# Optimization experiments

Measured on AMD Instinct MI355X. Metric: run time of the kernel, lower is better.

The kernel has to match this reference:

```python
import jax, jax.numpy as jnp
import numpy as np

N_HEAD = 6
NEG_INF = -1e9


def _structural_masks(adj, distance):
    """Build the 6 per-head structural masks (B, 6, L, L) bool.

    Heads: [self-loop only, 1-hop (adj), 2-hop reachable, distance<=2,
            distance<=3, global]. Inferred from the 6-signal docstring;
    preprocess_adj adds self loops and binarizes.
    """
    B, L, _ = adj.shape
    eye = jnp.eye(L, dtype=bool)[None]                      # (1, L, L)
    a1 = (adj > 0) | eye                                    # 1-hop + self
    a1f = a1.astype(jnp.float32)
    a2 = (jnp.einsum('blm,bmn->bln', a1f, a1f) > 0)         # 2-hop reachable
    d2 = distance <= 2
    d3 = distance <= 3
    full = jnp.ones((B, L, L), dtype=bool)
    return jnp.stack([jnp.broadcast_to(eye, (B, L, L)), a1, a2, d2, d3, full], axis=1)


def setup_inputs() -> dict:
    key = jax.random.key(0)
    k1, k2, k3, k4, k5 = jax.random.split(key, 5)
    B, L, C = 8, 1024, 768
    x = jax.random.normal(k1, (B, L, C), dtype=jnp.float32)
    adj = jax.random.randint(k2, (B, L, L), 0, 2, dtype=jnp.int32)
    distance = jax.random.randint(k3, (B, L, L), 0, 9, dtype=jnp.int32)
    w_qkv = jax.random.normal(k4, (3 * C, C), dtype=jnp.float32) * 0.02
    w_proj = jax.random.normal(k5, (C, C), dtype=jnp.float32) * 0.02
    return {"x": x, "adj": adj, "distance": distance, "w_qkv": w_qkv, "w_proj": w_proj}


def reference(x, adj, distance, w_qkv, w_proj):
    B, L, C = x.shape
    H = N_HEAD
    d = C // H
    scale = jnp.sqrt(jnp.float32(d))

    qkv = x @ w_qkv.T                                       # (B, L, 3C)
    q, k, v = jnp.split(qkv, 3, axis=-1)
    q = q.reshape(B, L, H, d).transpose(0, 2, 1, 3)         # (B, H, L, d)
    k = k.reshape(B, L, H, d).transpose(0, 2, 1, 3)
    v = v.reshape(B, L, H, d).transpose(0, 2, 1, 3)

    score = jnp.einsum('bhld,bhmd->bhlm', q, k) / scale     # (B, H, L, L)
    pe = _structural_masks(adj, distance)                   # (B, H, L, L) bool
    score = jnp.where(pe, score, NEG_INF)                   # masked_fill of bias
    attn = jax.nn.softmax(score, axis=-1)
    out = jnp.einsum('bhlm,bhmd->bhld', attn, v)            # (B, H, L, d)
    out = out.transpose(0, 2, 1, 3).reshape(B, L, C)
    return out @ w_proj.T
```

## Files before the change

### kernel.cpp

```cpp
#include <hip/hip_runtime.h>

typedef unsigned short ushort_t;
typedef unsigned int uint_t;
typedef unsigned long long u64;
typedef __attribute__((ext_vector_type(8))) short bf16x8;
typedef __attribute__((ext_vector_type(4))) float f32x4;
typedef __attribute__((ext_vector_type(16))) float f32x16;
typedef __attribute__((ext_vector_type(4))) uint_t u32x4;

#define B_ 8
#define L_ 1024
#define C_ 768
#define H_ 6
#define D_ 128
#define BH_ 48
#define NEGINF (-1e9f)
#define THR_ 8.0f

#define AS1 __attribute__((address_space(1)))
#define AS3 __attribute__((address_space(3)))

__device__ __forceinline__ ushort_t f2bf(float f) {
  uint_t u = __builtin_bit_cast(uint_t, f);
  u += 0x7fffu + ((u >> 16) & 1u);
  return (ushort_t)(u >> 16);
}
__device__ __forceinline__ float bf2f(ushort_t s) {
  uint_t u = ((uint_t)s) << 16;
  return __builtin_bit_cast(float, u);
}

__global__ void cvt_f32_bf16(const float* __restrict__ in, ushort_t* __restrict__ out, int n8) {
  int i = blockIdx.x * 256 + threadIdx.x;
  if (i >= n8) return;
  const float4* p = (const float4*)in + (size_t)i * 2;
  float4 a = p[0], b = p[1];
  uint4 r;
  r.x = (uint_t)f2bf(a.x) | ((uint_t)f2bf(a.y) << 16);
  r.y = (uint_t)f2bf(a.z) | ((uint_t)f2bf(a.w) << 16);
  r.z = (uint_t)f2bf(b.x) | ((uint_t)f2bf(b.y) << 16);
  r.w = (uint_t)f2bf(b.z) | ((uint_t)f2bf(b.w) << 16);
  ((uint4*)out)[i] = r;
}

__global__ __launch_bounds__(256)
void pack_masks(const int* __restrict__ adj, const int* __restrict__ dist,
                u64* __restrict__ a1p, u64* __restrict__ d2p, u64* __restrict__ d3p) {
  int l = blockIdx.x, b = blockIdx.y, t = threadIdx.x;
  size_t base = ((size_t)b * L_ + l) * L_;
  size_t rb = ((size_t)b * L_ + l) * 16;
  #pragma unroll
  for (int it = 0; it < 4; ++it) {
    int c = it * 256 + t;
    int av = adj[base + c];
    int dv = dist[base + c];
    u64 m1 = __ballot((av > 0) || (c == l));
    u64 m2 = __ballot(dv <= 2);
    u64 m3 = __ballot(dv <= 3);
    if ((t & 63) == 0) {
      int w = it * 4 + (t >> 6);
      a1p[rb + w] = m1; d2p[rb + w] = m2; d3p[rb + w] = m3;
    }
  }
}

__global__ __launch_bounds__(64)
void hop2(const u64* __restrict__ a1p, u64* __restrict__ a2p) {
  int tid = blockIdx.x * 64 + threadIdx.x;
  int b = tid >> 10;
  size_t rb = (size_t)tid * 16;
  u64 row[16], acc[16];
  #pragma unroll
  for (int j = 0; j < 16; ++j) { row[j] = a1p[rb + j]; acc[j] = 0ULL; }
  bool done = false;
  #pragma unroll
  for (int mw = 0; mw < 16; ++mw) {
    if (done) continue;
    u64 bits = row[mw];
    while (bits) {
      int tz = __builtin_ctzll(bits); bits &= bits - 1;
      const u64* src = a1p + (((size_t)b << 10) + (mw << 6) + tz) * 16;
      u64 band = ~0ULL;
      #pragma unroll
      for (int j = 0; j < 16; ++j) { acc[j] |= src[j]; band &= acc[j]; }
      if (band == ~0ULL) { done = true; break; }
    }
  }
  #pragma unroll
  for (int j = 0; j < 16; ++j) a2p[rb + j] = acc[j];
}

template<int EPI>
__global__ __launch_bounds__(256)
void gemm_bt(const ushort_t* __restrict__ A, const ushort_t* __restrict__ Bm,
             int N, int K,
             ushort_t* __restrict__ qo, ushort_t* __restrict__ ko,
             ushort_t* __restrict__ vTo, ushort_t* __restrict__ vo,
             float* __restrict__ fo) {
  __shared__ __align__(16) ushort_t As[128 * 64];
  __shared__ __align__(16) ushort_t Bs[128 * 64];
  int t = threadIdx.x;
  int lane = t & 63, lo = lane & 15, hi = lane >> 4;
  int wv = t >> 6, wm = wv >> 1, wn = wv & 1;

  int gx = gridDim.x;
  int nwg = gx * gridDim.y;
  int orig = blockIdx.y * gx + blockIdx.x;
  int cpx = nwg >> 3;
  int wg = (orig & 7) * cpx + (orig >> 3);
  int n0 = (wg % gx) * 128;
  int m0 = (wg / gx) * 128;

  f32x4 acc[4][4];
  #pragma unroll
  for (int mi = 0; mi < 4; ++mi)
    #pragma unroll
    for (int ni = 0; ni < 4; ++ni) acc[mi][ni] = (f32x4){0.f, 0.f, 0.f, 0.f};

  for (int kt = 0; kt < K; kt += 64) {
    #pragma unroll
    for (int i = 0; i < 4; ++i) {
      int u = i * 256 + t;
      int row = u >> 3, c16 = u & 7;
      int sc = c16 ^ (row & 7);
      __builtin_amdgcn_global_load_lds(
          (const AS1 void*)(A + ((size_t)(m0 + row) * K + kt + sc * 8)),
          (AS3 void*)&As[(size_t)u * 8], 16, 0, 0);
      __builtin_amdgcn_global_load_lds(
          (const AS1 void*)(Bm + ((size_t)(n0 + row) * K + kt + sc * 8)),
          (AS3 void*)&Bs[(size_t)u * 8], 16, 0, 0);
    }
    __syncthreads();
    #pragma unroll
    for (int kks = 0; kks < 2; ++kks) {
      bf16x8 af[4], bfr[4];
      #pragma unroll
      for (int mi = 0; mi < 4; ++mi) {
        int r = wm * 64 + mi * 16 + lo;
        af[mi] = *(const bf16x8*)&As[r * 64 + (((kks * 4 + hi) ^ (r & 7)) * 8)];
      }
      #pragma unroll
      for (int ni = 0; ni < 4; ++ni) {
        int r = wn * 64 + ni * 16 + lo;
        bfr[ni] = *(const bf16x8*)&Bs[r * 64 + (((kks * 4 + hi) ^ (r & 7)) * 8)];
      }
      #pragma unroll
      for (int mi = 0; mi < 4; ++mi)
        #pragma unroll
        for (int ni = 0; ni < 4; ++ni)
          acc[mi][ni] = __builtin_amdgcn_mfma_f32_16x16x32_bf16(af[mi], bfr[ni], acc[mi][ni], 0, 0, 0);
    }
    __syncthreads();
  }

  if (EPI == 1) {
    #pragma unroll
    for (int mi = 0; mi < 4; ++mi) {
      int rbase = m0 + wm * 64 + mi * 16 + hi * 4;
      #pragma unroll
      for (int ni = 0; ni < 4; ++ni) {
        int c = n0 + wn * 64 + ni * 16 + lo;
        f32x4 v = acc[mi][ni];
        #pragma unroll
        for (int j = 0; j < 4; ++j)
          fo[(size_t)(rbase + j) * N + c] = v[j];
      }
    }
    return;
  }
  int sec = n0 / 768;
  if (sec < 2) {
    #pragma unroll
    for (int mi = 0; mi < 4; ++mi) {
      int rbase = m0 + wm * 64 + mi * 16 + hi * 4;
      #pragma unroll
      for (int ni = 0; ni < 4; ++ni) {
        int cc = n0 - sec * 768 + wn * 64 + ni * 16 + lo;
        int hh = cc >> 7, dd = cc & 127;
        f32x4 v = acc[mi][ni];
        #pragma unroll
        for (int j = 0; j < 4; ++j) {
          int r = rbase + j;
          int b = r >> 10, l = r & 1023;
          size_t bh = (size_t)(b * H_ + hh);
          if (sec == 0) qo[(bh * L_ + l) * D_ + dd] = f2bf(v[j] * 0.08838834764831845f);
          else          ko[(bh * L_ + l) * D_ + dd] = f2bf(v[j]);
        }
      }
    }
    return;
  }
  int hh = (n0 - 1536) >> 7;
  int b = m0 >> 10, l0 = m0 & 1023;
  size_t bh = (size_t)(b * H_ + hh);
  if (hh == 0) {
    #pragma unroll
    for (int mi = 0; mi < 4; ++mi) {
      int lb = wm * 64 + mi * 16 + hi * 4;
      #pragma unroll
      for (int ni = 0; ni < 4; ++ni) {
        int dd = wn * 64 + ni * 16 + lo;
        f32x4 v = acc[mi][ni];
        #pragma unroll
        for (int j = 0; j < 4; ++j)
          vo[(bh * L_ + l0 + lb + j) * D_ + dd] = f2bf(v[j]);
      }
    }
    return;
  }
  #pragma unroll
  for (int mi = 0; mi < 4; ++mi) {
    int lb = wm * 64 + mi * 16 + hi * 4;
    #pragma unroll
    for (int ni = 0; ni < 4; ++ni) {
      int dd = wn * 64 + ni * 16 + lo;
      ushort_t* base = (dd < 64) ? As : Bs;
      f32x4 v = acc[mi][ni];
      #pragma unroll
      for (int j = 0; j < 4; ++j) {
        int byte = (((dd & 63) * 256 + (lb + j) * 2)) ^ ((dd & 7) << 4);
        *(ushort_t*)((char*)base + byte) = f2bf(v[j]);
      }
    }
  }
  __syncthreads();
  #pragma unroll
  for (int i = 0; i < 8; ++i) {
    int u = i * 256 + t;
    int ddl = u >> 4, c16 = u & 15;
    const ushort_t* base = (ddl < 64) ? As : Bs;
    int byte = (((ddl & 63) * 256 + c16 * 16)) ^ ((ddl & 7) << 4);
    bf16x8 val = *(const bf16x8*)((const char*)base + byte);
    *(bf16x8*)(vTo + (bh * D_ + ddl) * L_ + l0 + c16 * 8) = val;
  }
}

__global__ __launch_bounds__(512)
void attn_kernel(const ushort_t* __restrict__ q, const ushort_t* __restrict__ k,
                 const ushort_t* __restrict__ vT, const ushort_t* __restrict__ v,
                 ushort_t* __restrict__ obf,
                 ushort_t* __restrict__ np0, ushort_t* __restrict__ np1,
                 ushort_t* __restrict__ np2, ushort_t* __restrict__ np3,
                 float* __restrict__ ml,
                 const u64* __restrict__ a1p, const u64* __restrict__ a2p,
                 const u64* __restrict__ d2p, const u64* __restrict__ d3p) {
  __shared__ __align__(16) ushort_t Ks[2][32 * 128];
  __shared__ __align__(16) ushort_t Vs[2][128 * 32];
  int t = threadIdx.x;
  int lane = t & 63, lo32 = lane & 31, hi2 = (lane >> 5) & 1, wv = t >> 6;
  int bh = blockIdx.x, qt = blockIdx.y, quar = blockIdx.z;
  int b = bh / H_, h = bh - b * H_;
  int qbase = qt * 256;
  int qw = qbase + wv * 32;
  int kvb = quar * 256;

  if (h == 0) {
    if (quar) return;
    const ushort_t* vp0 = v + ((size_t)bh * L_ + qbase) * D_;
    ushort_t* op0 = obf + ((size_t)b * L_ + qbase) * C_;
    #pragma unroll
    for (int it = 0; it < 8; ++it) {
      int u = it * 512 + t;
      int r = u >> 4, c = (u & 15) * 8;
      *(bf16x8*)(op0 + (size_t)r * C_ + c) = *(const bf16x8*)(vp0 + (size_t)r * D_ + c);
    }
    return;
  }

  const ushort_t* qp = q + (size_t)bh * L_ * D_;
  const ushort_t* kp = k + (size_t)bh * L_ * D_ + (size_t)kvb * D_;
  const ushort_t* vp = vT + (size_t)bh * D_ * L_ + kvb;

  bf16x8 qf[8];
  #pragma unroll
  for (int dt = 0; dt < 8; ++dt)
    qf[dt] = *(const bf16x8*)(qp + (size_t)(qw + lo32) * D_ + dt * 16 + hi2 * 8);

  const u64* mp = (h == 1) ? a1p : (h == 2) ? a2p : (h == 3) ? d2p : d3p;
  bool full = (h == 5);
  const u64* mrow = mp + ((size_t)b * L_ + qw + lo32) * 16 + quar * 4;

  float m_run = NEGINF, l_run = 0.f;
  f32x16 acc[4];
  #pragma unroll
  for (int dt = 0; dt < 4; ++dt)
    #pragma unroll
    for (int r = 0; r < 16; ++r) acc[dt][r] = 0.f;

  auto stage = [&](int buf, int ch) {
    int kc0 = ch * 32;
    {
      int row = t >> 4, c16 = t & 15;
      int sc = c16 ^ (row & 15);
      __builtin_amdgcn_global_load_lds(
          (const AS1 void*)(kp + (size_t)(kc0 + row) * D_ + sc * 8),
          (AS3 void*)&Ks[buf][(size_t)t * 8], 16, 0, 0);
    }
    {
      int row = t >> 2, c16 = t & 3;
      int sc = c16 ^ (row & 3);
      __builtin_amdgcn_global_load_lds(
          (const AS1 void*)(vp + (size_t)row * L_ + kc0 + sc * 8),
          (AS3 void*)&Vs[buf][(size_t)t * 8], 16, 0, 0);
    }
  };

  stage(0, 0);
  u64 mw_cur = full ? 0ULL : mrow[0];
  u64 mw_nxt = 0ULL;
  __syncthreads();

  for (int ch = 0; ch < 8; ++ch) {
    int cur = ch & 1;
    if (ch < 7) stage(cur ^ 1, ch + 1);
    if (!full && (ch & 1) == 0 && (ch >> 1) + 1 < 4)
      mw_nxt = mrow[(ch >> 1) + 1];

    const ushort_t* ks = &Ks[cur][0];
    const ushort_t* vs = &Vs[cur][0];
    uint_t mbits = full ? 0xffffffffu : (uint_t)(mw_cur >> ((ch & 1) * 32));

    f32x16 sacc;
    #pragma unroll
    for (int r = 0; r < 16; ++r) sacc[r] = 0.f;
    __builtin_amdgcn_s_setprio(1);
    #pragma unroll
    for (int dt = 0; dt < 8; ++dt) {
      int c16 = (dt * 2 + hi2) ^ (lo32 & 15);
      bf16x8 kf = *(const bf16x8*)&ks[lo32 * 128 + c16 * 8];
      sacc = __builtin_amdgcn_mfma_f32_32x32x16_bf16(kf, qf[dt], sacc, 0, 0, 0);
    }
    __builtin_amdgcn_s_setprio(0);

    float sv[16];
    #pragma unroll
    for (int r = 0; r < 16; ++r) {
      int shift = (r & 3) + 8 * (r >> 2) + hi2 * 4;
      sv[r] = ((mbits >> shift) & 1u) ? sacc[r] : NEGINF;
    }

    float a8[8];
    #pragma unroll
    for (int j = 0; j < 8; ++j) a8[j] = fmaxf(sv[2 * j], sv[2 * j + 1]);
    #pragma unroll
    for (int j = 0; j < 4; ++j) a8[j] = fmaxf(a8[j], a8[j + 4]);
    float pmax = fmaxf(fmaxf(a8[0], a8[1]), fmaxf(a8[2], a8[3]));
    pmax = fmaxf(pmax, __shfl_xor(pmax, 32));

    if (__any(pmax > m_run + THR_)) {
      float mn = fmaxf(m_run, pmax);
      float corr = __expf(m_run - mn);
      l_run *= corr;
      m_run = mn;
      float cT[16];
      #pragma unroll
      for (int r = 0; r < 16; ++r)
        cT[r] = __shfl(corr, (r & 3) + 8 * (r >> 2) + hi2 * 4);
      #pragma unroll
      for (int dt = 0; dt < 4; ++dt)
        #pragma unroll
        for (int r = 0; r < 16; ++r) acc[dt][r] *= cT[r];
    }

    float p[16];
    #pragma unroll
    for (int r = 0; r < 16; ++r) p[r] = __expf(sv[r] - m_run);
    float s8[8];
    #pragma unroll
    for (int j = 0; j < 8; ++j) s8[j] = p[2 * j] + p[2 * j + 1];
    #pragma unroll
    for (int j = 0; j < 4; ++j) s8[j] = s8[j] + s8[j + 4];
    float rs = (s8[0] + s8[1]) + (s8[2] + s8[3]);
    rs += __shfl_xor(rs, 32);
    l_run += rs;

    uint_t ow[8];
    #pragma unroll
    for (int j = 0; j < 8; ++j)
      ow[j] = (uint_t)f2bf(p[2 * j]) | ((uint_t)f2bf(p[2 * j + 1]) << 16);
    uint_t pw[8];
    #pragma unroll
    for (int j = 0; j < 8; ++j) pw[j] = __shfl_xor(ow[j], 32);
    u32x4 pa0 = (u32x4){hi2 ? pw[2] : ow[0], hi2 ? pw[3] : ow[1],
                        hi2 ? ow[2] : pw[0], hi2 ? ow[3] : pw[1]};
    u32x4 pa1 = (u32x4){hi2 ? pw[6] : ow[4], hi2 ? pw[7] : ow[5],
                        hi2 ? ow[6] : pw[4], hi2 ? ow[7] : pw[5]};
    bf16x8 paf0 = __builtin_bit_cast(bf16x8, pa0);
    bf16x8 paf1 = __builtin_bit_cast(bf16x8, pa1);

    __builtin_amdgcn_s_setprio(1);
    #pragma unroll
    for (int dt = 0; dt < 4; ++dt) {
      int vd = dt * 32 + lo32;
      int c16a = hi2 ^ (vd & 3);
      int c16b = (2 + hi2) ^ (vd & 3);
      bf16x8 vfa = *(const bf16x8*)&vs[vd * 32 + c16a * 8];
      bf16x8 vfb = *(const bf16x8*)&vs[vd * 32 + c16b * 8];
      acc[dt] = __builtin_amdgcn_mfma_f32_32x32x16_bf16(paf0, vfa, acc[dt], 0, 0, 0);
      acc[dt] = __builtin_amdgcn_mfma_f32_32x32x16_bf16(paf1, vfb, acc[dt], 0, 0, 0);
    }
    __builtin_amdgcn_s_setprio(0);
    if (ch & 1) mw_cur = mw_nxt;
    __syncthreads();
  }

  if (hi2 == 0) {
    size_t row = (size_t)bh * L_ + qw + lo32;
    float2 v2 = make_float2(m_run, l_run);
    *(float2*)(ml + ((size_t)quar * BH_ * L_ + row) * 2) = v2;
  }
  ushort_t* np = (quar == 0) ? np0 : (quar == 1) ? np1 : (quar == 2) ? np2 : np3;
  #pragma unroll
  for (int dt = 0; dt < 4; ++dt)
    #pragma unroll
    for (int r = 0; r < 16; ++r) {
      int qrow = qw + (r & 3) + 8 * (r >> 2) + hi2 * 4;
      np[((size_t)bh * L_ + qrow) * D_ + dt * 32 + lo32] = f2bf(acc[dt][r]);
    }
}

__global__ __launch_bounds__(256)
void combine(const ushort_t* __restrict__ np0, const ushort_t* __restrict__ np1,
             const ushort_t* __restrict__ np2, const ushort_t* __restrict__ np3,
             const float* __restrict__ ml, ushort_t* __restrict__ obf) {
  int bh = blockIdx.x;
  int b = bh / H_, h = bh - b * H_;
  if (h == 0) return;
  int t = threadIdx.x;
  int qi = t >> 4, di = t & 15;
  int qq = blockIdx.y * 16 + qi;
  size_t row = (size_t)bh * L_ + qq;
  float2 mlv[4];
  #pragma unroll
  for (int s = 0; s < 4; ++s)
    mlv[s] = *(const float2*)(ml + ((size_t)s * BH_ * L_ + row) * 2);
  float M = fmaxf(fmaxf(mlv[0].x, mlv[1].x), fmaxf(mlv[2].x, mlv[3].x));
  float w[4], lsum = 0.f;
  #pragma unroll
  for (int s = 0; s < 4; ++s) { w[s] = __expf(mlv[s].x - M); lsum += w[s] * mlv[s].y; }
  float inv = 1.f / lsum;
  bf16x8 n0 = *(const bf16x8*)(np0 + row * D_ + di * 8);
  bf16x8 n1 = *(const bf16x8*)(np1 + row * D_ + di * 8);
  bf16x8 n2 = *(const bf16x8*)(np2 + row * D_ + di * 8);
  bf16x8 n3 = *(const bf16x8*)(np3 + row * D_ + di * 8);
  ushort_t o[8];
  #pragma unroll
  for (int j = 0; j < 8; ++j)
    o[j] = f2bf((w[0] * bf2f((ushort_t)n0[j]) + w[1] * bf2f((ushort_t)n1[j]) +
                 w[2] * bf2f((ushort_t)n2[j]) + w[3] * bf2f((ushort_t)n3[j])) * inv);
  *(bf16x8*)(obf + ((size_t)b * L_ + qq) * C_ + h * D_ + di * 8) = *(bf16x8*)o;
}

extern "C" void kernel_launch(void* const* d_in, const int* in_sizes, int n_in,
                              void* d_out, int out_size, void* d_ws, size_t ws_size,
                              hipStream_t stream) {
  const float* x     = (const float*)d_in[0];
  const int*   adj   = (const int*)d_in[1];
  const int*   dist  = (const int*)d_in[2];
  const float* wqkv  = (const float*)d_in[3];
  const float* wproj = (const float*)d_in[4];
  float* out = (float*)d_out;
  char* ws = (char*)d_ws;

  const size_t SZ_X   = (size_t)B_ * L_ * C_ * 2;
  const size_t SZ_WQ  = (size_t)3 * C_ * C_ * 2;
  const size_t SZ_WP  = (size_t)C_ * C_ * 2;
  const size_t SZ_QKV = (size_t)BH_ * L_ * D_ * 2;
  const size_t SZ_MSK = (size_t)B_ * L_ * 16 * 8;
  const size_t SZ_ML  = (size_t)4 * BH_ * L_ * 2 * 4;
  size_t off = 0;
  ushort_t* xbf  = (ushort_t*)(ws + off); off += SZ_X;
  ushort_t* wqb  = (ushort_t*)(ws + off); off += SZ_WQ;
  ushort_t* wpb  = (ushort_t*)(ws + off); off += SZ_WP;
  ushort_t* qb   = (ushort_t*)(ws + off); off += SZ_QKV;
  ushort_t* kb   = (ushort_t*)(ws + off); off += SZ_QKV;
  ushort_t* vTb  = (ushort_t*)(ws + off); off += SZ_QKV;
  ushort_t* vb   = (ushort_t*)(ws + off); off += SZ_QKV;
  ushort_t* ob   = (ushort_t*)(ws + off); off += SZ_X;
  u64* a1p = (u64*)(ws + off); off += SZ_MSK;
  u64* a2p = (u64*)(ws + off); off += SZ_MSK;
  u64* d2p = (u64*)(ws + off); off += SZ_MSK;
  u64* d3p = (u64*)(ws + off); off += SZ_MSK;
  ushort_t* np1 = (ushort_t*)(ws + off); off += SZ_QKV;
  ushort_t* np2 = (ushort_t*)(ws + off); off += SZ_QKV;
  ushort_t* np3 = (ushort_t*)(ws + off); off += SZ_QKV;
  float*    mlb = (float*)(ws + off); off += SZ_ML;
  ushort_t* np0 = xbf;
  (void)ws_size; (void)n_in; (void)in_sizes; (void)out_size;

  cvt_f32_bf16<<<(B_ * L_ * C_ / 8 + 255) / 256, 256, 0, stream>>>(x, xbf, B_ * L_ * C_ / 8);
  cvt_f32_bf16<<<(3 * C_ * C_ / 8 + 255) / 256, 256, 0, stream>>>(wqkv, wqb, 3 * C_ * C_ / 8);
  cvt_f32_bf16<<<(C_ * C_ / 8 + 255) / 256, 256, 0, stream>>>(wproj, wpb, C_ * C_ / 8);
  pack_masks<<<dim3(L_, B_), 256, 0, stream>>>(adj, dist, a1p, d2p, d3p);
  hop2<<<B_ * L_ / 64, 64, 0, stream>>>(a1p, a2p);
  gemm_bt<0><<<dim3(3 * C_ / 128, B_ * L_ / 128), 256, 0, stream>>>(
      xbf, wqb, 3 * C_, C_, qb, kb, vTb, vb, nullptr);
  attn_kernel<<<dim3(BH_, L_ / 256, 4), 512, 0, stream>>>(
      qb, kb, vTb, vb, ob, np0, np1, np2, np3, mlb, a1p, a2p, d2p, d3p);
  combine<<<dim3(BH_, L_ / 16), 256, 0, stream>>>(np0, np1, np2, np3, mlb, ob);
  gemm_bt<1><<<dim3(C_ / 128, B_ * L_ / 128), 256, 0, stream>>>(
      ob, wpb, C_, C_, nullptr, nullptr, nullptr, nullptr, out);
}
```

Baseline: 179.9 us.

## Process two query tiles per wave to reuse staged K/V tiles

Each attention block now covers 512 query rows instead of 256, so every wave handles two 32-row query tiles against the same K/V chunk in LDS. The first tile's Q fragments stay in registers. The second tile's Q is staged into a new 64KB shared buffer and re-read from LDS every chunk. This halves K/V global traffic and staging per query row, but it doubles accumulator registers, raises LDS per block, and halves the grid. That can lower occupancy and worsen load balance across CUs.

```diff
diff --git a/kernel.cpp b/kernel.cpp
--- a/kernel.cpp
+++ b/kernel.cpp
@@ -246,11 +246,12 @@
                  const u64* __restrict__ d2p, const u64* __restrict__ d3p) {
   __shared__ __align__(16) ushort_t Ks[2][32 * 128];
   __shared__ __align__(16) ushort_t Vs[2][128 * 32];
+  __shared__ __align__(16) ushort_t Qs[8][32 * 128];
   int t = threadIdx.x;
   int lane = t & 63, lo32 = lane & 31, hi2 = (lane >> 5) & 1, wv = t >> 6;
   int bh = blockIdx.x, qt = blockIdx.y, quar = blockIdx.z;
   int b = bh / H_, h = bh - b * H_;
-  int qbase = qt * 256;
+  int qbase = qt * 512;
   int qw = qbase + wv * 32;
   int kvb = quar * 256;
 
@@ -259,7 +260,7 @@
     const ushort_t* vp0 = v + ((size_t)bh * L_ + qbase) * D_;
     ushort_t* op0 = obf + ((size_t)b * L_ + qbase) * C_;
     #pragma unroll
-    for (int it = 0; it < 8; ++it) {
+    for (int it = 0; it < 16; ++it) {
       int u = it * 512 + t;
       int r = u >> 4, c = (u & 15) * 8;
       *(bf16x8*)(op0 + (size_t)r * C_ + c) = *(const bf16x8*)(vp0 + (size_t)r * D_ + c);
@@ -271,21 +272,33 @@
   const ushort_t* kp = k + (size_t)bh * L_ * D_ + (size_t)kvb * D_;
   const ushort_t* vp = vT + (size_t)bh * D_ * L_ + kvb;
 
-  bf16x8 qf[8];
+  #pragma unroll
+  for (int i = 0; i < 8; ++i) {
+    int u = i * 64 + lane;
+    int row = u >> 4, c16 = u & 15;
+    int sc = c16 ^ (row & 15);
+    __builtin_amdgcn_global_load_lds(
+        (const AS1 void*)(qp + (size_t)(qw + 256 + row) * D_ + sc * 8),
+        (AS3 void*)&Qs[wv][(size_t)u * 8], 16, 0, 0);
+  }
+  bf16x8 qf0[8];
   #pragma unroll
   for (int dt = 0; dt < 8; ++dt)
-    qf[dt] = *(const bf16x8*)(qp + (size_t)(qw + lo32) * D_ + dt * 16 + hi2 * 8);
+    qf0[dt] = *(const bf16x8*)(qp + (size_t)(qw + lo32) * D_ + dt * 16 + hi2 * 8);
 
   const u64* mp = (h == 1) ? a1p : (h == 2) ? a2p : (h == 3) ? d2p : d3p;
   bool full = (h == 5);
-  const u64* mrow = mp + ((size_t)b * L_ + qw + lo32) * 16 + quar * 4;
-
-  float m_run = NEGINF, l_run = 0.f;
-  f32x16 acc[4];
-  #pragma unroll
-  for (int dt = 0; dt < 4; ++dt)
-    #pragma unroll
-    for (int r = 0; r < 16; ++r) acc[dt][r] = 0.f;
+  const u64* mrow0 = mp + ((size_t)b * L_ + qw + lo32) * 16 + quar * 4;
+  const u64* mrow1 = mrow0 + (size_t)256 * 16;
+
+  float m_run[2] = {NEGINF, NEGINF}, l_run[2] = {0.f, 0.f};
+  f32x16 acc[2][4];
+  #pragma unroll
+  for (int tl = 0; tl < 2; ++tl)
+    #pragma unroll
+    for (int dt = 0; dt < 4; ++dt)
+      #pragma unroll
+      for (int r = 0; r < 16; ++r) acc[tl][dt][r] = 0.f;
 
   auto stage = [&](int buf, int ch) {
     int kc0 = ch * 32;
@@ -306,87 +319,96 @@
   };
 
   stage(0, 0);
-  u64 mw_cur = full ? 0ULL : mrow[0];
-  u64 mw_nxt = 0ULL;
+  u64 mw_cur[2] = {0, 0}, mw_nxt[2] = {0, 0};
+  if (!full) { mw_cur[0] = mrow0[0]; mw_cur[1] = mrow1[0]; }
   __syncthreads();
 
   for (int ch = 0; ch < 8; ++ch) {
     int cur = ch & 1;
     if (ch < 7) stage(cur ^ 1, ch + 1);
-    if (!full && (ch & 1) == 0 && (ch >> 1) + 1 < 4)
-      mw_nxt = mrow[(ch >> 1) + 1];
+    if (!full && (ch & 1) == 0 && (ch >> 1) + 1 < 4) {
+      mw_nxt[0] = mrow0[(ch >> 1) + 1];
+      mw_nxt[1] = mrow1[(ch >> 1) + 1];
+    }
 
     const ushort_t* ks = &Ks[cur][0];
     const ushort_t* vs = &Vs[cur][0];
-    uint_t mbits = full ? 0xffffffffu : (uint_t)(mw_cur >> ((ch & 1) * 32));
-
-    f32x16 sacc;
-    #pragma unroll
-    for (int r = 0; r < 16; ++r) sacc[r] = 0.f;
-    __builtin_amdgcn_s_setprio(1);
-    #pragma unroll
-    for (int dt = 0; dt < 8; ++dt) {
-      int c16 = (dt * 2 + hi2) ^ (lo32 & 15);
-      bf16x8 kf = *(const bf16x8*)&ks[lo32 * 128 + c16 * 8];
-      sacc = __builtin_amdgcn_mfma_f32_32x32x16_bf16(kf, qf[dt], sacc, 0, 0, 0);
-    }
-    __builtin_amdgcn_s_setprio(0);
-
-    float sv[16];
-    #pragma unroll
-    for (int r = 0; r < 16; ++r) {
-      int shift = (r & 3) + 8 * (r >> 2) + hi2 * 4;
-      sv[r] = ((mbits >> shift) & 1u) ? sacc[r] : NEGINF;
-    }
-
-    float a8[8];
-    #pragma unroll
-    for (int j = 0; j < 8; ++j) a8[j] = fmaxf(sv[2 * j], sv[2 * j + 1]);
-    #pragma unroll
-    for (int j = 0; j < 4; ++j) a8[j] = fmaxf(a8[j], a8[j + 4]);
-    float pmax = fmaxf(fmaxf(a8[0], a8[1]), fmaxf(a8[2], a8[3]));
-    pmax = fmaxf(pmax, __shfl_xor(pmax, 32));
-
-    if (__any(pmax > m_run + THR_)) {
-      float mn = fmaxf(m_run, pmax);
-      float corr = __expf(m_run - mn);
-      l_run *= corr;
-      m_run = mn;
-      float cT[16];
-      #pragma unroll
-      for (int r = 0; r < 16; ++r)
-        cT[r] = __shfl(corr, (r & 3) + 8 * (r >> 2) + hi2 * 4);
-      #pragma unroll
-      for (int dt = 0; dt < 4; ++dt)
+
+    bf16x8 paf[2][2];
+    #pragma unroll
+    for (int tl = 0; tl < 2; ++tl) {
+      f32x16 sacc;
+      #pragma unroll
+      for (int r = 0; r < 16; ++r) sacc[r] = 0.f;
+      __builtin_amdgcn_s_setprio(1);
+      #pragma unroll
+      for (int dt = 0; dt < 8; ++dt) {
+        int c16 = (dt * 2 + hi2) ^ (lo32 & 15);
+        bf16x8 kf = *(const bf16x8*)&ks[lo32 * 128 + c16 * 8];
+        bf16x8 qd;
+        if (tl == 0) qd = qf0[dt];
+        else         qd = *(const bf16x8*)&Qs[wv][lo32 * 128 + c16 * 8];
+        sacc = __builtin_amdgcn_mfma_f32_32x32x16_bf16(kf, qd, sacc, 0, 0, 0);
+      }
+      __builtin_amdgcn_s_setprio(0);
+
+      uint_t mbits = full ? 0xffffffffu : (uint_t)(mw_cur[tl] >> ((ch & 1) * 32));
+      float sv[16];
+      #pragma unroll
+      for (int r = 0; r < 16; ++r) {
+        int shift = (r & 3) + 8 * (r >> 2) + hi2 * 4;
+        sv[r] = ((mbits >> shift) & 1u) ? sacc[r] : NEGINF;
+      }
+
+      float a8[8];
+      #pragma unroll
+      for (int j = 0; j < 8; ++j) a8[j] = fmaxf(sv[2 * j], sv[2 * j + 1]);
+      #pragma unroll
+      for (int j = 0; j < 4; ++j) a8[j] = fmaxf(a8[j], a8[j + 4]);
+      float pmax = fmaxf(fmaxf(a8[0], a8[1]), fmaxf(a8[2], a8[3]));
+      pmax = fmaxf(pmax, __shfl_xor(pmax, 32));
+
+      if (__any(pmax > m_run[tl] + THR_)) {
+        float mn = fmaxf(m_run[tl], pmax);
+        float corr = __expf(m_run[tl] - mn);
+        l_run[tl] *= corr;
+        m_run[tl] = mn;
+        float cT[16];
         #pragma unroll
-        for (int r = 0; r < 16; ++r) acc[dt][r] *= cT[r];
-    }
-
-    float p[16];
-    #pragma unroll
-    for (int r = 0; r < 16; ++r) p[r] = __expf(sv[r] - m_run);
-    float s8[8];
-    #pragma unroll
-    for (int j = 0; j < 8; ++j) s8[j] = p[2 * j] + p[2 * j + 1];
-    #pragma unroll
-    for (int j = 0; j < 4; ++j) s8[j] = s8[j] + s8[j + 4];
-    float rs = (s8[0] + s8[1]) + (s8[2] + s8[3]);
-    rs += __shfl_xor(rs, 32);
-    l_run += rs;
-
-    uint_t ow[8];
-    #pragma unroll
-    for (int j = 0; j < 8; ++j)
-      ow[j] = (uint_t)f2bf(p[2 * j]) | ((uint_t)f2bf(p[2 * j + 1]) << 16);
-    uint_t pw[8];
-    #pragma unroll
-    for (int j = 0; j < 8; ++j) pw[j] = __shfl_xor(ow[j], 32);
-    u32x4 pa0 = (u32x4){hi2 ? pw[2] : ow[0], hi2 ? pw[3] : ow[1],
-                        hi2 ? ow[2] : pw[0], hi2 ? ow[3] : pw[1]};
-    u32x4 pa1 = (u32x4){hi2 ? pw[6] : ow[4], hi2 ? pw[7] : ow[5],
-                        hi2 ? ow[6] : pw[4], hi2 ? ow[7] : pw[5]};
-    bf16x8 paf0 = __builtin_bit_cast(bf16x8, pa0);
-    bf16x8 paf1 = __builtin_bit_cast(bf16x8, pa1);
+        for (int r = 0; r < 16; ++r)
+          cT[r] = __shfl(corr, (r & 3) + 8 * (r >> 2) + hi2 * 4);
+        #pragma unroll
+        for (int dt = 0; dt < 4; ++dt)
+          #pragma unroll
+          for (int r = 0; r < 16; ++r) acc[tl][dt][r] *= cT[r];
+      }
+
+      float p[16];
+      #pragma unroll
+      for (int r = 0; r < 16; ++r) p[r] = __expf(sv[r] - m_run[tl]);
+      float s8[8];
+      #pragma unroll
+      for (int j = 0; j < 8; ++j) s8[j] = p[2 * j] + p[2 * j + 1];
+      #pragma unroll
+      for (int j = 0; j < 4; ++j) s8[j] = s8[j] + s8[j + 4];
+      float rs = (s8[0] + s8[1]) + (s8[2] + s8[3]);
+      rs += __shfl_xor(rs, 32);
+      l_run[tl] += rs;
+
+      uint_t ow[8];
+      #pragma unroll
+      for (int j = 0; j < 8; ++j)
+        ow[j] = (uint_t)f2bf(p[2 * j]) | ((uint_t)f2bf(p[2 * j + 1]) << 16);
+      uint_t pw[8];
+      #pragma unroll
+      for (int j = 0; j < 8; ++j) pw[j] = __shfl_xor(ow[j], 32);
+      u32x4 pa0 = (u32x4){hi2 ? pw[2] : ow[0], hi2 ? pw[3] : ow[1],
+                          hi2 ? ow[2] : pw[0], hi2 ? ow[3] : pw[1]};
+      u32x4 pa1 = (u32x4){hi2 ? pw[6] : ow[4], hi2 ? pw[7] : ow[5],
+                          hi2 ? ow[6] : pw[4], hi2 ? ow[7] : pw[5]};
+      paf[tl][0] = __builtin_bit_cast(bf16x8, pa0);
+      paf[tl][1] = __builtin_bit_cast(bf16x8, pa1);
+    }
 
     __builtin_amdgcn_s_setprio(1);
     #pragma unroll
@@ -396,27 +418,33 @@
       int c16b = (2 + hi2) ^ (vd & 3);
       bf16x8 vfa = *(const bf16x8*)&vs[vd * 32 + c16a * 8];
       bf16x8 vfb = *(const bf16x8*)&vs[vd * 32 + c16b * 8];
-      acc[dt] = __builtin_amdgcn_mfma_f32_32x32x16_bf16(paf0, vfa, acc[dt], 0, 0, 0);
-      acc[dt] = __builtin_amdgcn_mfma_f32_32x32x16_bf16(paf1, vfb, acc[dt], 0, 0, 0);
+      acc[0][dt] = __builtin_amdgcn_mfma_f32_32x32x16_bf16(paf[0][0], vfa, acc[0][dt], 0, 0, 0);
+      acc[0][dt] = __builtin_amdgcn_mfma_f32_32x32x16_bf16(paf[0][1], vfb, acc[0][dt], 0, 0, 0);
+      acc[1][dt] = __builtin_amdgcn_mfma_f32_32x32x16_bf16(paf[1][0], vfa, acc[1][dt], 0, 0, 0);
+      acc[1][dt] = __builtin_amdgcn_mfma_f32_32x32x16_bf16(paf[1][1], vfb, acc[1][dt], 0, 0, 0);
     }
     __builtin_amdgcn_s_setprio(0);
-    if (ch & 1) mw_cur = mw_nxt;
+    if (ch & 1) { mw_cur[0] = mw_nxt[0]; mw_cur[1] = mw_nxt[1]; }
     __syncthreads();
   }
 
-  if (hi2 == 0) {
-    size_t row = (size_t)bh * L_ + qw + lo32;
-    float2 v2 = make_float2(m_run, l_run);
-    *(float2*)(ml + ((size_t)quar * BH_ * L_ + row) * 2) = v2;
-  }
   ushort_t* np = (quar == 0) ? np0 : (quar == 1) ? np1 : (quar == 2) ? np2 : np3;
   #pragma unroll
-  for (int dt = 0; dt < 4; ++dt)
-    #pragma unroll
-    for (int r = 0; r < 16; ++r) {
-      int qrow = qw + (r & 3) + 8 * (r >> 2) + hi2 * 4;
-      np[((size_t)bh * L_ + qrow) * D_ + dt * 32 + lo32] = f2bf(acc[dt][r]);
-    }
+  for (int tl = 0; tl < 2; ++tl) {
+    int qb2 = qw + tl * 256;
+    if (hi2 == 0) {
+      size_t row = (size_t)bh * L_ + qb2 + lo32;
+      float2 v2 = make_float2(m_run[tl], l_run[tl]);
+      *(float2*)(ml + ((size_t)quar * BH_ * L_ + row) * 2) = v2;
+    }
+    #pragma unroll
+    for (int dt = 0; dt < 4; ++dt)
+      #pragma unroll
+      for (int r = 0; r < 16; ++r) {
+        int qrow = qb2 + (r & 3) + 8 * (r >> 2) + hi2 * 4;
+        np[((size_t)bh * L_ + qrow) * D_ + dt * 32 + lo32] = f2bf(acc[tl][dt][r]);
+      }
+  }
 }
 
 __global__ __launch_bounds__(256)
@@ -495,7 +523,7 @@
   hop2<<<B_ * L_ / 64, 64, 0, stream>>>(a1p, a2p);
   gemm_bt<0><<<dim3(3 * C_ / 128, B_ * L_ / 128), 256, 0, stream>>>(
       xbf, wqb, 3 * C_, C_, qb, kb, vTb, vb, nullptr);
-  attn_kernel<<<dim3(BH_, L_ / 256, 4), 512, 0, stream>>>(
+  attn_kernel<<<dim3(BH_, L_ / 512, 4), 512, 0, stream>>>(
       qb, kb, vTb, vb, ob, np0, np1, np2, np3, mlb, a1p, a2p, d2p, d3p);
   combine<<<dim3(BH_, L_ / 16), 256, 0, stream>>>(np0, np1, np2, np3, mlb, ob);
   gemm_bt<1><<<dim3(C_ / 128, B_ * L_ / 128), 256, 0, stream>>>(
```

Result: slower. 201.6 us (+12.1%).
